# Optimization experiments

Hardware: AMD Instinct MI355X
Metric: run time of the kernel (lower is better)

## Reference

```python
import jax, jax.numpy as jnp
import numpy as np

NUM_HEADS = 4


def setup_inputs() -> dict:
    key = jax.random.key(0)
    ks = jax.random.split(key, 5)
    B, C, L = 8, 128, 2048
    x = jax.random.normal(ks[0], (B, C, L), dtype=jnp.float32)
    # Conv1d(C, 3C, 1) == per-position linear; weight [3C, C], bias [3C]
    w_qkv = jax.random.normal(ks[1], (3 * C, C), dtype=jnp.float32) * (1.0 / np.sqrt(C))
    b_qkv = jax.random.normal(ks[2], (3 * C,), dtype=jnp.float32) * 0.01
    w_proj = jax.random.normal(ks[3], (C, C), dtype=jnp.float32) * (1.0 / np.sqrt(C))
    b_proj = jax.random.normal(ks[4], (C,), dtype=jnp.float32) * 0.01
    return {"x": x, "w_qkv": w_qkv, "b_qkv": b_qkv, "w_proj": w_proj, "b_proj": b_proj}


def reference(x, w_qkv, b_qkv, w_proj, b_proj):
    B, C, L = x.shape
    H = NUM_HEADS
    D = C // H
    scale = D ** -0.5
    # 1x1 conv qkv projection: [B, 3C, L]
    qkv = jnp.einsum('oc,bcl->bol', w_qkv, x) + b_qkv[None, :, None]
    # reshape (B,3,H,D,L) -> permute to (3,B,H,L,D)
    qkv = qkv.reshape(B, 3, H, D, L).transpose(1, 0, 2, 4, 3)
    q, k, v = qkv[0], qkv[1], qkv[2]  # each [B, H, L, D]
    attn = jax.nn.softmax(jnp.einsum('bhld,bhmd->bhlm', q, k) * scale, axis=-1)
    out = jnp.einsum('bhlm,bhmd->bhld', attn, v)  # [B, H, L, D]
    out = out.transpose(0, 1, 3, 2).reshape(B, C, L)
    out = jnp.einsum('oc,bcl->bol', w_proj, out) + b_proj[None, :, None]
    return out + x
```

## Files before the change

kernel.cpp:

```cpp
#include <hip/hip_runtime.h>

#define Bsz 8
#define Cdim 128
#define Lseq 2048
#define NH 4
#define HD 32
#define BH 32
#define QSCALE (0.17677669529663687f * 1.4426950408889634f)

typedef __bf16 bf16x8 __attribute__((ext_vector_type(8)));
typedef __bf16 bf16x4 __attribute__((ext_vector_type(4)));
typedef float f32x4 __attribute__((ext_vector_type(4)));
typedef unsigned u32x4 __attribute__((ext_vector_type(4)));

__device__ __forceinline__ float fexp2(float x) {
#if __has_builtin(__builtin_amdgcn_exp2f)
    return __builtin_amdgcn_exp2f(x);
#else
    return __expf(x * 0.6931471805599453f);
#endif
}

__device__ __forceinline__ unsigned short f2bf(float f) {
    unsigned u = __builtin_bit_cast(unsigned, f);
    u += 0x7FFFu + ((u >> 16) & 1u);
    return (unsigned short)(u >> 16);
}

__device__ __forceinline__ unsigned pack_bf16(float a, float b) {
    return (unsigned)f2bf(a) | ((unsigned)f2bf(b) << 16);
}

__device__ __forceinline__ unsigned pack_bf16_rtz(float a, float b) {
    return __builtin_amdgcn_perm(__builtin_bit_cast(unsigned, b),
                                 __builtin_bit_cast(unsigned, a), 0x07060302u);
}

__device__ __forceinline__ float bf_lo(unsigned u) {
    return __builtin_bit_cast(float, u << 16);
}
__device__ __forceinline__ float bf_hi(unsigned u) {
    return __builtin_bit_cast(float, u & 0xFFFF0000u);
}

#define MFMA16(A, B, C) __builtin_amdgcn_mfma_f32_16x16x32_bf16((A), (B), (C), 0, 0, 0)

__global__ __launch_bounds__(256) void qkv_kernel(const float* __restrict__ x,
        const float* __restrict__ w, const float* __restrict__ bias,
        unsigned short* __restrict__ qh, unsigned short* __restrict__ kh,
        unsigned short* __restrict__ vh) {
    __shared__ __attribute__((aligned(16))) unsigned short T[64][132];
    int bid = blockIdx.x;
    int b  = bid >> 5;
    int l0 = (bid & 31) * 64;
    int t = threadIdx.x;
    int lane = t & 63, wv = t >> 6;
    int m16 = lane & 15, quad = lane >> 4;
    int o0w = wv * 96;

    bf16x8 af[6][4];
    #pragma unroll
    for (int os = 0; os < 6; os++) {
        const float* wr = w + (size_t)(o0w + os * 16 + m16) * Cdim;
        #pragma unroll
        for (int ks = 0; ks < 4; ks++) {
            const float* p = wr + ks * 32 + quad * 8;
            float4 f0 = *(const float4*)p;
            float4 f1 = *(const float4*)(p + 4);
            u32x4 u = {pack_bf16(f0.x, f0.y), pack_bf16(f0.z, f0.w),
                       pack_bf16(f1.x, f1.y), pack_bf16(f1.z, f1.w)};
            af[os][ks] = __builtin_bit_cast(bf16x8, u);
        }
    }

    {
        int l = t & 63, cg = t >> 6;
        const float* xb = x + (size_t)b * Cdim * Lseq + l0 + l;
        #pragma unroll
        for (int i = 0; i < 16; i++) {
            int c = cg * 32 + 2 * i;
            float f0 = xb[(size_t)c * Lseq];
            float f1 = xb[(size_t)(c + 1) * Lseq];
            *(unsigned*)&T[l][c] = pack_bf16(f0, f1);
        }
    }

    float bs[6][4];
    #pragma unroll
    for (int os = 0; os < 6; os++)
        #pragma unroll
        for (int r = 0; r < 4; r++)
            bs[os][r] = bias[o0w + os * 16 + quad * 4 + r];

    __syncthreads();

    #pragma unroll
    for (int ns = 0; ns < 4; ns++) {
        bf16x8 bx[4];
        #pragma unroll
        for (int ks = 0; ks < 4; ks++)
            bx[ks] = *(const bf16x8*)(&T[ns * 16 + m16][ks * 32 + quad * 8]);
        int l = l0 + ns * 16 + m16;
        int kc = l >> 6, kk = l & 63;
        #pragma unroll
        for (int os = 0; os < 6; os++) {
            f32x4 acc = {0.f, 0.f, 0.f, 0.f};
            #pragma unroll
            for (int ks = 0; ks < 4; ks++) acc = MFMA16(af[os][ks], bx[ks], acc);
            int o0s = o0w + os * 16 + quad * 4;
            if (o0s < Cdim) {
                int h = o0s >> 5, d0 = o0s & 31;
                uint2 u;
                u.x = pack_bf16((acc[0] + bs[os][0]) * QSCALE, (acc[1] + bs[os][1]) * QSCALE);
                u.y = pack_bf16((acc[2] + bs[os][2]) * QSCALE, (acc[3] + bs[os][3]) * QSCALE);
                *(uint2*)(qh + ((size_t)(b * NH + h) * Lseq + l) * HD + d0) = u;
            } else if (o0s < 2 * Cdim) {
                int o = o0s - Cdim, h = o >> 5, d0 = o & 31;
                uint2 u;
                u.x = pack_bf16(acc[0] + bs[os][0], acc[1] + bs[os][1]);
                u.y = pack_bf16(acc[2] + bs[os][2], acc[3] + bs[os][3]);
                *(uint2*)(kh + ((size_t)(b * NH + h) * Lseq + l) * HD + d0) = u;
            } else {
                #pragma unroll
                for (int r = 0; r < 4; r++) {
                    int o = o0s + r - 2 * Cdim, h = o >> 5, d = o & 31;
                    vh[(((size_t)(b * NH + h) * 32 + kc) * HD + d) * 64 + kk] =
                        f2bf(acc[r] + bs[os][r]);
                }
            }
        }
    }
}

__global__ __launch_bounds__(256) void attn_kernel(
        const unsigned short* __restrict__ qh, const unsigned short* __restrict__ kh,
        const unsigned short* __restrict__ vh, unsigned short* __restrict__ attnb) {
    __shared__ __attribute__((aligned(16))) char smem[19456];

    int bid = blockIdx.x;
    int xcd  = bid & 7;
    int rest = bid >> 3;
    int qt = rest & 31;
    int bh = xcd + 8 * (rest >> 5);

    int lane = threadIdx.x & 63;
    int wv   = threadIdx.x >> 6;
    int m16  = lane & 15;
    int quad = lane >> 4;
    int l0 = qt * 64;

    bf16x8 qf[4];
    #pragma unroll
    for (int qs = 0; qs < 4; qs++)
        qf[qs] = *(const bf16x8*)(qh + ((size_t)bh * Lseq + l0 + qs * 16 + m16) * HD + quad * 8);

    bf16x8 ones;
    #pragma unroll
    for (int i = 0; i < 8; i++) ones[i] = (__bf16)1.0f;

    f32x4 oacc[4][2];
    f32x4 lacc[4];
    #pragma unroll
    for (int qs = 0; qs < 4; qs++) {
        oacc[qs][0] = f32x4{0.f, 0.f, 0.f, 0.f};
        oacc[qs][1] = f32x4{0.f, 0.f, 0.f, 0.f};
        lacc[qs]    = f32x4{0.f, 0.f, 0.f, 0.f};
    }
    f32x4 zero = {0.f, 0.f, 0.f, 0.f};

    const unsigned short* kb = kh + (size_t)bh * Lseq * HD + m16 * HD + quad * 8;
    const unsigned short* vb = vh + (size_t)bh * 32 * HD * 64;

    bf16x8 kf[4], vf[4], kfN[4], vfN[4];
    {
        int k0 = wv * 512;
        #pragma unroll
        for (int t = 0; t < 4; t++)
            kf[t] = *(const bf16x8*)(kb + (size_t)(k0 + 16 * t) * HD);
        const unsigned short* vch = vb + (size_t)(k0 >> 6) * (HD * 64);
        const unsigned short* vrl = vch + m16 * 64 + 4 * quad;
        const unsigned short* vrh = vch + (16 + m16) * 64 + 4 * quad;
        bf16x4 a0 = *(const bf16x4*)(vrl),      a1 = *(const bf16x4*)(vrl + 16);
        bf16x4 a2 = *(const bf16x4*)(vrl + 32), a3 = *(const bf16x4*)(vrl + 48);
        bf16x4 b0 = *(const bf16x4*)(vrh),      b1 = *(const bf16x4*)(vrh + 16);
        bf16x4 b2 = *(const bf16x4*)(vrh + 32), b3 = *(const bf16x4*)(vrh + 48);
        vf[0] = __builtin_shufflevector(a0, a1, 0, 1, 2, 3, 4, 5, 6, 7);
        vf[1] = __builtin_shufflevector(b0, b1, 0, 1, 2, 3, 4, 5, 6, 7);
        vf[2] = __builtin_shufflevector(a2, a3, 0, 1, 2, 3, 4, 5, 6, 7);
        vf[3] = __builtin_shufflevector(b2, b3, 0, 1, 2, 3, 4, 5, 6, 7);
    }

    for (int it = 0; it < 8; it++) {
        int nx = it < 7 ? it + 1 : 7;
        {
            int k0 = wv * 512 + nx * 64;
            #pragma unroll
            for (int t = 0; t < 4; t++)
                kfN[t] = *(const bf16x8*)(kb + (size_t)(k0 + 16 * t) * HD);
            const unsigned short* vch = vb + (size_t)(k0 >> 6) * (HD * 64);
            const unsigned short* vrl = vch + m16 * 64 + 4 * quad;
            const unsigned short* vrh = vch + (16 + m16) * 64 + 4 * quad;
            bf16x4 a0 = *(const bf16x4*)(vrl),      a1 = *(const bf16x4*)(vrl + 16);
            bf16x4 a2 = *(const bf16x4*)(vrl + 32), a3 = *(const bf16x4*)(vrl + 48);
            bf16x4 b0 = *(const bf16x4*)(vrh),      b1 = *(const bf16x4*)(vrh + 16);
            bf16x4 b2 = *(const bf16x4*)(vrh + 32), b3 = *(const bf16x4*)(vrh + 48);
            vfN[0] = __builtin_shufflevector(a0, a1, 0, 1, 2, 3, 4, 5, 6, 7);
            vfN[1] = __builtin_shufflevector(b0, b1, 0, 1, 2, 3, 4, 5, 6, 7);
            vfN[2] = __builtin_shufflevector(a2, a3, 0, 1, 2, 3, 4, 5, 6, 7);
            vfN[3] = __builtin_shufflevector(b2, b3, 0, 1, 2, 3, 4, 5, 6, 7);
        }

        #pragma unroll
        for (int qs = 0; qs < 4; qs++) {
            f32x4 s0 = MFMA16(kf[0], qf[qs], zero);
            f32x4 s1 = MFMA16(kf[1], qf[qs], zero);
            f32x4 s2 = MFMA16(kf[2], qf[qs], zero);
            f32x4 s3 = MFMA16(kf[3], qf[qs], zero);
            float p00 = fexp2(s0[0]), p01 = fexp2(s0[1]), p02 = fexp2(s0[2]), p03 = fexp2(s0[3]);
            float p10 = fexp2(s1[0]), p11 = fexp2(s1[1]), p12 = fexp2(s1[2]), p13 = fexp2(s1[3]);
            float p20 = fexp2(s2[0]), p21 = fexp2(s2[1]), p22 = fexp2(s2[2]), p23 = fexp2(s2[3]);
            float p30 = fexp2(s3[0]), p31 = fexp2(s3[1]), p32 = fexp2(s3[2]), p33 = fexp2(s3[3]);
            u32x4 lo = {pack_bf16_rtz(p00, p01), pack_bf16_rtz(p02, p03),
                        pack_bf16_rtz(p10, p11), pack_bf16_rtz(p12, p13)};
            u32x4 hi = {pack_bf16_rtz(p20, p21), pack_bf16_rtz(p22, p23),
                        pack_bf16_rtz(p30, p31), pack_bf16_rtz(p32, p33)};
            bf16x8 pfL = __builtin_bit_cast(bf16x8, lo);
            bf16x8 pfH = __builtin_bit_cast(bf16x8, hi);
            oacc[qs][0] = MFMA16(vf[0], pfL, oacc[qs][0]);
            oacc[qs][1] = MFMA16(vf[1], pfL, oacc[qs][1]);
            lacc[qs]    = MFMA16(ones,  pfL, lacc[qs]);
            oacc[qs][0] = MFMA16(vf[2], pfH, oacc[qs][0]);
            oacc[qs][1] = MFMA16(vf[3], pfH, oacc[qs][1]);
            lacc[qs]    = MFMA16(ones,  pfH, lacc[qs]);
        }
        #pragma unroll
        for (int t = 0; t < 4; t++) { kf[t] = kfN[t]; vf[t] = vfN[t]; }
    }

    unsigned* red_o = (unsigned*)smem;
    float* red_l = (float*)(smem + 18432);
    #pragma unroll
    for (int qs = 0; qs < 4; qs++) {
        int row = qs * 16 + m16;
        unsigned* rw = red_o + (size_t)(wv * 64 + row) * 18;
        *(uint2*)(rw + 2 * quad) =
            make_uint2(pack_bf16_rtz(oacc[qs][0][0], oacc[qs][0][1]),
                       pack_bf16_rtz(oacc[qs][0][2], oacc[qs][0][3]));
        *(uint2*)(rw + 8 + 2 * quad) =
            make_uint2(pack_bf16_rtz(oacc[qs][1][0], oacc[qs][1][1]),
                       pack_bf16_rtz(oacc[qs][1][2], oacc[qs][1][3]));
        if (quad == 0) red_l[wv * 64 + row] = lacc[qs][0];
    }
    __syncthreads();

    int q = threadIdx.x >> 2;
    int s4 = (threadIdx.x & 3) * 4;
    float a8[8] = {0.f, 0.f, 0.f, 0.f, 0.f, 0.f, 0.f, 0.f};
    float lt = 0.f;
    #pragma unroll
    for (int w = 0; w < 4; w++) {
        const unsigned* rr = red_o + (size_t)(w * 64 + q) * 18 + s4;
        uint2 ua = *(const uint2*)(rr);
        uint2 ub = *(const uint2*)(rr + 2);
        a8[0] += bf_lo(ua.x); a8[1] += bf_hi(ua.x);
        a8[2] += bf_lo(ua.y); a8[3] += bf_hi(ua.y);
        a8[4] += bf_lo(ub.x); a8[5] += bf_hi(ub.x);
        a8[6] += bf_lo(ub.y); a8[7] += bf_hi(ub.y);
        lt += red_l[w * 64 + q];
    }
    float inv = 1.0f / lt;
    int b = bh >> 2, h = bh & 3;
    int d0 = (threadIdx.x & 3) * 8;
    unsigned short* ob = attnb + ((size_t)b * Lseq + l0 + q) * Cdim + h * HD + d0;
    uint4 u;
    u.x = pack_bf16(a8[0] * inv, a8[1] * inv);
    u.y = pack_bf16(a8[2] * inv, a8[3] * inv);
    u.z = pack_bf16(a8[4] * inv, a8[5] * inv);
    u.w = pack_bf16(a8[6] * inv, a8[7] * inv);
    *(uint4*)ob = u;
}

__global__ __launch_bounds__(256) void proj_kernel(const float* __restrict__ wp,
        const unsigned short* __restrict__ attnb, const float* __restrict__ bias,
        const float* __restrict__ x, float* __restrict__ out) {
    int bid = blockIdx.x;
    int ot = bid & 1;
    int nt = bid >> 1;
    int lane = threadIdx.x & 63;
    int wv = threadIdx.x >> 6;
    int m16 = lane & 15, quad = lane >> 4;
    int o0 = ot * 64 + wv * 16;
    int n0 = nt * 64;

    bf16x8 af[4];
    #pragma unroll
    for (int ks = 0; ks < 4; ks++) {
        const float* p = wp + (size_t)(o0 + m16) * Cdim + ks * 32 + quad * 8;
        float4 f0 = *(const float4*)p;
        float4 f1 = *(const float4*)(p + 4);
        u32x4 u = {pack_bf16(f0.x, f0.y), pack_bf16(f0.z, f0.w),
                   pack_bf16(f1.x, f1.y), pack_bf16(f1.z, f1.w)};
        af[ks] = __builtin_bit_cast(bf16x8, u);
    }
    float bs[4];
    #pragma unroll
    for (int r = 0; r < 4; r++) bs[r] = bias[o0 + quad * 4 + r];
    int oq = o0 + quad * 4;

    for (int lt2 = 0; lt2 < 4; lt2++) {
        int n = n0 + lt2 * 16 + m16;
        f32x4 acc = {0.f, 0.f, 0.f, 0.f};
        #pragma unroll
        for (int ks = 0; ks < 4; ks++) {
            bf16x8 bx = *(const bf16x8*)(attnb + (size_t)n * Cdim + ks * 32 + quad * 8);
            acc = MFMA16(af[ks], bx, acc);
        }
        int b = n >> 11, l = n & (Lseq - 1);
        #pragma unroll
        for (int r = 0; r < 4; r++) {
            size_t xi = ((size_t)b * Cdim + oq + r) * Lseq + l;
            out[xi] = acc[r] + bs[r] + x[xi];
        }
    }
}

extern "C" void kernel_launch(void* const* d_in, const int* in_sizes, int n_in,
                              void* d_out, int out_size, void* d_ws, size_t ws_size,
                              hipStream_t stream) {
    const float* x      = (const float*)d_in[0];
    const float* w_qkv  = (const float*)d_in[1];
    const float* b_qkv  = (const float*)d_in[2];
    const float* w_proj = (const float*)d_in[3];
    const float* b_proj = (const float*)d_in[4];
    float* out = (float*)d_out;

    const size_t E = (size_t)BH * Lseq * HD;
    unsigned short* qh    = (unsigned short*)d_ws;
    unsigned short* kh    = qh + E;
    unsigned short* vh    = kh + E;
    unsigned short* attnb = vh + E;

    qkv_kernel<<<dim3(256), dim3(256), 0, stream>>>(x, w_qkv, b_qkv, qh, kh, vh);
    attn_kernel<<<dim3(BH * 32), dim3(256), 0, stream>>>(qh, kh, vh, attnb);
    proj_kernel<<<dim3(512), dim3(256), 0, stream>>>(w_proj, attnb, b_proj, x, out);
}
```

Before: 131.2 us.

## Split QKV and proj grids, permute V layout, double-buffer K/V in attention

The QKV kernel now splits the output channels across 6 blocks per position tile, giving 1536 blocks instead of 256 and fewer registers per block. The V layout is permuted when written so the attention kernel can fetch each V fragment with one 16-byte load instead of two 8-byte loads and a shuffle. The attention loop is rewritten as an unrolled ping-pong double buffer. The projection kernel gets half the work per block and twice as many blocks. The cost is that each QKV block now reloads and transposes the same x tile, six times over in total.

```diff
diff --git a/kernel.cpp b/kernel.cpp
--- a/kernel.cpp
+++ b/kernel.cpp
@@ -9,7 +9,6 @@
 #define QSCALE (0.17677669529663687f * 1.4426950408889634f)
 
 typedef __bf16 bf16x8 __attribute__((ext_vector_type(8)));
-typedef __bf16 bf16x4 __attribute__((ext_vector_type(4)));
 typedef float f32x4 __attribute__((ext_vector_type(4)));
 typedef unsigned u32x4 __attribute__((ext_vector_type(4)));
 
@@ -51,82 +50,77 @@
         unsigned short* __restrict__ vh) {
     __shared__ __attribute__((aligned(16))) unsigned short T[64][132];
     int bid = blockIdx.x;
-    int b  = bid >> 5;
-    int l0 = (bid & 31) * 64;
+    int og = bid % 6;
+    int lt = (bid / 6) & 31;
+    int b  = bid / 192;
+    int l0 = lt * 64;
     int t = threadIdx.x;
     int lane = t & 63, wv = t >> 6;
     int m16 = lane & 15, quad = lane >> 4;
-    int o0w = wv * 96;
-
-    bf16x8 af[6][4];
-    #pragma unroll
-    for (int os = 0; os < 6; os++) {
-        const float* wr = w + (size_t)(o0w + os * 16 + m16) * Cdim;
-        #pragma unroll
-        for (int ks = 0; ks < 4; ks++) {
-            const float* p = wr + ks * 32 + quad * 8;
-            float4 f0 = *(const float4*)p;
-            float4 f1 = *(const float4*)(p + 4);
-            u32x4 u = {pack_bf16(f0.x, f0.y), pack_bf16(f0.z, f0.w),
-                       pack_bf16(f1.x, f1.y), pack_bf16(f1.z, f1.w)};
-            af[os][ks] = __builtin_bit_cast(bf16x8, u);
-        }
-    }
+    int o0 = og * 64 + wv * 16;
+
+    bf16x8 af[4];
+    #pragma unroll
+    for (int ks = 0; ks < 4; ks++) {
+        const float* p = w + (size_t)(o0 + m16) * Cdim + ks * 32 + quad * 8;
+        float4 f0 = *(const float4*)p;
+        float4 f1 = *(const float4*)(p + 4);
+        u32x4 u = {pack_bf16(f0.x, f0.y), pack_bf16(f0.z, f0.w),
+                   pack_bf16(f1.x, f1.y), pack_bf16(f1.z, f1.w)};
+        af[ks] = __builtin_bit_cast(bf16x8, u);
+    }
+    float bs[4];
+    #pragma unroll
+    for (int r = 0; r < 4; r++) bs[r] = bias[o0 + quad * 4 + r];
 
     {
-        int l = t & 63, cg = t >> 6;
-        const float* xb = x + (size_t)b * Cdim * Lseq + l0 + l;
+        int ll = t & 63, cg = t >> 6;
+        const float* xb = x + (size_t)b * Cdim * Lseq + l0 + ll;
         #pragma unroll
         for (int i = 0; i < 16; i++) {
             int c = cg * 32 + 2 * i;
             float f0 = xb[(size_t)c * Lseq];
             float f1 = xb[(size_t)(c + 1) * Lseq];
-            *(unsigned*)&T[l][c] = pack_bf16(f0, f1);
-        }
-    }
-
-    float bs[6][4];
-    #pragma unroll
-    for (int os = 0; os < 6; os++)
-        #pragma unroll
-        for (int r = 0; r < 4; r++)
-            bs[os][r] = bias[o0w + os * 16 + quad * 4 + r];
-
+            *(unsigned*)&T[ll][c] = pack_bf16(f0, f1);
+        }
+    }
     __syncthreads();
 
+    int oq = o0 + quad * 4;
     #pragma unroll
     for (int ns = 0; ns < 4; ns++) {
         bf16x8 bx[4];
         #pragma unroll
         for (int ks = 0; ks < 4; ks++)
             bx[ks] = *(const bf16x8*)(&T[ns * 16 + m16][ks * 32 + quad * 8]);
+        f32x4 acc = {0.f, 0.f, 0.f, 0.f};
+        #pragma unroll
+        for (int ks = 0; ks < 4; ks++) acc = MFMA16(af[ks], bx[ks], acc);
         int l = l0 + ns * 16 + m16;
-        int kc = l >> 6, kk = l & 63;
-        #pragma unroll
-        for (int os = 0; os < 6; os++) {
-            f32x4 acc = {0.f, 0.f, 0.f, 0.f};
+        if (og < 2) {
+            int h = oq >> 5, d0 = oq & 31;
+            uint2 u;
+            u.x = pack_bf16((acc[0] + bs[0]) * QSCALE, (acc[1] + bs[1]) * QSCALE);
+            u.y = pack_bf16((acc[2] + bs[2]) * QSCALE, (acc[3] + bs[3]) * QSCALE);
+            *(uint2*)(qh + ((size_t)(b * NH + h) * Lseq + l) * HD + d0) = u;
+        } else if (og < 4) {
+            int o = oq - Cdim, h = o >> 5, d0 = o & 31;
+            uint2 u;
+            u.x = pack_bf16(acc[0] + bs[0], acc[1] + bs[1]);
+            u.y = pack_bf16(acc[2] + bs[2], acc[3] + bs[3]);
+            *(uint2*)(kh + ((size_t)(b * NH + h) * Lseq + l) * HD + d0) = u;
+        } else {
+            int kc = l >> 6, kk = l & 63;
+            int half = kk >> 5, k32 = kk & 31;
+            int q_, j_;
+            if (k32 < 16) { q_ = k32 >> 2; j_ = k32 & 3; }
+            else          { q_ = (k32 - 16) >> 2; j_ = 4 + ((k32 - 16) & 3); }
+            int pos = half * 32 + q_ * 8 + j_;
             #pragma unroll
-            for (int ks = 0; ks < 4; ks++) acc = MFMA16(af[os][ks], bx[ks], acc);
-            int o0s = o0w + os * 16 + quad * 4;
-            if (o0s < Cdim) {
-                int h = o0s >> 5, d0 = o0s & 31;
-                uint2 u;
-                u.x = pack_bf16((acc[0] + bs[os][0]) * QSCALE, (acc[1] + bs[os][1]) * QSCALE);
-                u.y = pack_bf16((acc[2] + bs[os][2]) * QSCALE, (acc[3] + bs[os][3]) * QSCALE);
-                *(uint2*)(qh + ((size_t)(b * NH + h) * Lseq + l) * HD + d0) = u;
-            } else if (o0s < 2 * Cdim) {
-                int o = o0s - Cdim, h = o >> 5, d0 = o & 31;
-                uint2 u;
-                u.x = pack_bf16(acc[0] + bs[os][0], acc[1] + bs[os][1]);
-                u.y = pack_bf16(acc[2] + bs[os][2], acc[3] + bs[os][3]);
-                *(uint2*)(kh + ((size_t)(b * NH + h) * Lseq + l) * HD + d0) = u;
-            } else {
-                #pragma unroll
-                for (int r = 0; r < 4; r++) {
-                    int o = o0s + r - 2 * Cdim, h = o >> 5, d = o & 31;
-                    vh[(((size_t)(b * NH + h) * 32 + kc) * HD + d) * 64 + kk] =
-                        f2bf(acc[r] + bs[os][r]);
-                }
+            for (int r = 0; r < 4; r++) {
+                int o = oq + r - 2 * Cdim, h = o >> 5, d = o & 31;
+                vh[(((size_t)(b * NH + h) * 32 + kc) * HD + d) * 64 + pos] =
+                    f2bf(acc[r] + bs[r]);
             }
         }
     }
@@ -170,46 +164,21 @@
 
     const unsigned short* kb = kh + (size_t)bh * Lseq * HD + m16 * HD + quad * 8;
     const unsigned short* vb = vh + (size_t)bh * 32 * HD * 64;
-
-    bf16x8 kf[4], vf[4], kfN[4], vfN[4];
-    {
-        int k0 = wv * 512;
+    int kbase = wv * 512;
+
+    auto load_kv = [&](int chunk, bf16x8* kf, bf16x8* vf) {
+        int k0 = kbase + chunk * 64;
         #pragma unroll
         for (int t = 0; t < 4; t++)
             kf[t] = *(const bf16x8*)(kb + (size_t)(k0 + 16 * t) * HD);
         const unsigned short* vch = vb + (size_t)(k0 >> 6) * (HD * 64);
-        const unsigned short* vrl = vch + m16 * 64 + 4 * quad;
-        const unsigned short* vrh = vch + (16 + m16) * 64 + 4 * quad;
-        bf16x4 a0 = *(const bf16x4*)(vrl),      a1 = *(const bf16x4*)(vrl + 16);
-        bf16x4 a2 = *(const bf16x4*)(vrl + 32), a3 = *(const bf16x4*)(vrl + 48);
-        bf16x4 b0 = *(const bf16x4*)(vrh),      b1 = *(const bf16x4*)(vrh + 16);
-        bf16x4 b2 = *(const bf16x4*)(vrh + 32), b3 = *(const bf16x4*)(vrh + 48);
-        vf[0] = __builtin_shufflevector(a0, a1, 0, 1, 2, 3, 4, 5, 6, 7);
-        vf[1] = __builtin_shufflevector(b0, b1, 0, 1, 2, 3, 4, 5, 6, 7);
-        vf[2] = __builtin_shufflevector(a2, a3, 0, 1, 2, 3, 4, 5, 6, 7);
-        vf[3] = __builtin_shufflevector(b2, b3, 0, 1, 2, 3, 4, 5, 6, 7);
-    }
-
-    for (int it = 0; it < 8; it++) {
-        int nx = it < 7 ? it + 1 : 7;
-        {
-            int k0 = wv * 512 + nx * 64;
-            #pragma unroll
-            for (int t = 0; t < 4; t++)
-                kfN[t] = *(const bf16x8*)(kb + (size_t)(k0 + 16 * t) * HD);
-            const unsigned short* vch = vb + (size_t)(k0 >> 6) * (HD * 64);
-            const unsigned short* vrl = vch + m16 * 64 + 4 * quad;
-            const unsigned short* vrh = vch + (16 + m16) * 64 + 4 * quad;
-            bf16x4 a0 = *(const bf16x4*)(vrl),      a1 = *(const bf16x4*)(vrl + 16);
-            bf16x4 a2 = *(const bf16x4*)(vrl + 32), a3 = *(const bf16x4*)(vrl + 48);
-            bf16x4 b0 = *(const bf16x4*)(vrh),      b1 = *(const bf16x4*)(vrh + 16);
-            bf16x4 b2 = *(const bf16x4*)(vrh + 32), b3 = *(const bf16x4*)(vrh + 48);
-            vfN[0] = __builtin_shufflevector(a0, a1, 0, 1, 2, 3, 4, 5, 6, 7);
-            vfN[1] = __builtin_shufflevector(b0, b1, 0, 1, 2, 3, 4, 5, 6, 7);
-            vfN[2] = __builtin_shufflevector(a2, a3, 0, 1, 2, 3, 4, 5, 6, 7);
-            vfN[3] = __builtin_shufflevector(b2, b3, 0, 1, 2, 3, 4, 5, 6, 7);
-        }
-
+        vf[0] = *(const bf16x8*)(vch + m16 * 64 + quad * 8);
+        vf[1] = *(const bf16x8*)(vch + (16 + m16) * 64 + quad * 8);
+        vf[2] = *(const bf16x8*)(vch + m16 * 64 + 32 + quad * 8);
+        vf[3] = *(const bf16x8*)(vch + (16 + m16) * 64 + 32 + quad * 8);
+    };
+
+    auto compute = [&](const bf16x8* kf, const bf16x8* vf) {
         #pragma unroll
         for (int qs = 0; qs < 4; qs++) {
             f32x4 s0 = MFMA16(kf[0], qf[qs], zero);
@@ -233,8 +202,17 @@
             oacc[qs][1] = MFMA16(vf[3], pfH, oacc[qs][1]);
             lacc[qs]    = MFMA16(ones,  pfH, lacc[qs]);
         }
-        #pragma unroll
-        for (int t = 0; t < 4; t++) { kf[t] = kfN[t]; vf[t] = vfN[t]; }
+    };
+
+    bf16x8 kA[4], vA[4], kB[4], vB[4];
+    load_kv(0, kA, vA);
+    load_kv(1, kB, vB);
+    #pragma unroll
+    for (int it = 0; it < 8; it += 2) {
+        compute(kA, vA);
+        load_kv(it + 2 < 8 ? it + 2 : 7, kA, vA);
+        compute(kB, vB);
+        load_kv(it + 3 < 8 ? it + 3 : 7, kB, vB);
     }
 
     unsigned* red_o = (unsigned*)smem;
@@ -290,7 +268,7 @@
     int wv = threadIdx.x >> 6;
     int m16 = lane & 15, quad = lane >> 4;
     int o0 = ot * 64 + wv * 16;
-    int n0 = nt * 64;
+    int n0 = nt * 32;
 
     bf16x8 af[4];
     #pragma unroll
@@ -307,7 +285,8 @@
     for (int r = 0; r < 4; r++) bs[r] = bias[o0 + quad * 4 + r];
     int oq = o0 + quad * 4;
 
-    for (int lt2 = 0; lt2 < 4; lt2++) {
+    #pragma unroll
+    for (int lt2 = 0; lt2 < 2; lt2++) {
         int n = n0 + lt2 * 16 + m16;
         f32x4 acc = {0.f, 0.f, 0.f, 0.f};
         #pragma unroll
@@ -340,7 +319,7 @@
     unsigned short* vh    = kh + E;
     unsigned short* attnb = vh + E;
 
-    qkv_kernel<<<dim3(256), dim3(256), 0, stream>>>(x, w_qkv, b_qkv, qh, kh, vh);
+    qkv_kernel<<<dim3(1536), dim3(256), 0, stream>>>(x, w_qkv, b_qkv, qh, kh, vh);
     attn_kernel<<<dim3(BH * 32), dim3(256), 0, stream>>>(qh, kh, vh, attnb);
-    proj_kernel<<<dim3(512), dim3(256), 0, stream>>>(w_proj, attnb, b_proj, x, out);
-}
+    proj_kernel<<<dim3(1024), dim3(256), 0, stream>>>(w_proj, attnb, b_proj, x, out);
+}
```

Result: faster. 121.2 us (-7.6%).
